# Performance work log

Hardware: AMD Instinct MI355X
Metric: run time of the kernel (lower is better)

The kernel has to match this reference:

```python
import jax, jax.numpy as jnp
import numpy as np

N = 10000      # nodes
E = 640000     # edges
P = 500000     # OD training pairs
IN, HID, EMB = 128, 256, 64


def _graph_conv(x, W, b, src, dst, norm_out, norm_in):
    # DGL GraphConv, norm='both': y = D_in^{-1/2} A (D_out^{-1/2} x) W + b
    h = x * norm_out[:, None]
    agg = jax.ops.segment_sum(h[src], dst, num_segments=N)  # [N, d]
    return agg * norm_in[:, None] @ W + b


def setup_inputs() -> dict:
    key = jax.random.key(0)
    ks = jax.random.split(key, 13)
    x = jax.random.normal(ks[0], (N, IN), jnp.float32)
    dis = jax.random.uniform(ks[1], (N, N), jnp.float32)
    src = jax.random.randint(ks[2], (E,), 0, N, dtype=jnp.int64)
    dst = jax.random.randint(ks[3], (E,), 0, N, dtype=jnp.int64)
    train_idx = jax.random.randint(ks[4], (2, P), 0, N, dtype=jnp.int64)

    def w(k, i, o):
        return (jax.random.normal(k, (i, o), jnp.float32) / np.sqrt(i)).astype(jnp.float32)

    return {
        'x': x, 'dis': dis,
        'W1': w(ks[5], IN, HID),  'b1': jnp.zeros((HID,), jnp.float32),
        'W2': w(ks[6], HID, HID), 'b2': jnp.zeros((HID,), jnp.float32),
        'W3': w(ks[7], HID, EMB), 'b3': jnp.zeros((EMB,), jnp.float32),
        'Wout': w(ks[8], 2 * EMB + 1, 1), 'bout': jnp.zeros((1,), jnp.float32),
        'src': src, 'dst': dst, 'train_idx': train_idx,
    }


def reference(x, dis, W1, b1, W2, b2, W3, b3, Wout, bout, src, dst, train_idx):
    ones = jnp.ones((E,), x.dtype)
    deg_out = jax.ops.segment_sum(ones, src, num_segments=N)
    deg_in = jax.ops.segment_sum(ones, dst, num_segments=N)
    norm_out = jnp.where(deg_out > 0, jax.lax.rsqrt(jnp.maximum(deg_out, 1.0)), 0.0)
    norm_in = jnp.where(deg_in > 0, jax.lax.rsqrt(jnp.maximum(deg_in, 1.0)), 0.0)

    h = jax.nn.relu(_graph_conv(x, W1, b1, src, dst, norm_out, norm_in))
    h = jax.nn.relu(_graph_conv(h, W2, b2, src, dst, norm_out, norm_in))
    g_emb = jax.nn.sigmoid(_graph_conv(h, W3, b3, src, dst, norm_out, norm_in))  # [N, EMB]

    o_emb = g_emb[train_idx[0]]                      # [P, EMB]
    d_emb = g_emb[train_idx[1]]                      # [P, EMB]
    dis_emb = dis[train_idx[0], train_idx[1]][:, None]  # [P, 1]
    emb = jnp.concatenate((o_emb, d_emb, dis_emb), axis=1)  # [P, 2*EMB+1]
    return jnp.tanh(emb @ Wout + bout)               # [P, 1]
```

## Files before the change

### kernel.cpp

```cpp
#include <hip/hip_runtime.h>
#include <math.h>

typedef __attribute__((ext_vector_type(8))) short short8;
typedef __attribute__((ext_vector_type(8))) unsigned short ushort8;
typedef __attribute__((ext_vector_type(4))) float f32x4;

#define NTHR 256
#define CAP 192

__device__ __forceinline__ ushort f2bf(float f) {
    uint u = __float_as_uint(f);
    return (ushort)((u + 0x7FFFu + ((u >> 16) & 1u)) >> 16);
}
__device__ __forceinline__ uint pk2bf(float a, float b) {
    return (uint)f2bf(a) | ((uint)f2bf(b) << 16);
}
__device__ __forceinline__ float bfl(uint r) { return __uint_as_float(r << 16); }
__device__ __forceinline__ float bfh(uint r) { return __uint_as_float(r & 0xFFFF0000u); }

struct Params {
    const float* x; const float* dis;
    const float* W1; const float* b1;
    const float* W2; const float* b2;
    const float* W3; const float* b3;
    const float* Wout; const float* bout;
    const int* src; const int* dst; const int* ti;
    float* out;
    uint* degOut; uint* fill;
    float* normOut; float* normIn;
    ushort* ebkt;
    ushort* xbf; ushort* w1bf; ushort* w2bf; ushort* w3bf;
    ushort* bufA; ushort* bufB; ushort* bufC;
    float* av; float* bv;
    int N, E, P;
};

__global__ __launch_bounds__(NTHR) void k_pre(Params p) {
    int gtid = blockIdx.x * NTHR + threadIdx.x;
    int GSZ = gridDim.x * NTHR;
    for (int i = gtid; i < p.N; i += GSZ) {
        p.degOut[i] = 0u;
        p.fill[i] = 0u;
    }
    if (gtid < 64) ((uint*)&p.xbf[(size_t)p.N * 128])[gtid] = 0u;
    else if (gtid < 192) ((uint*)&p.bufB[(size_t)p.N * 256])[gtid - 64] = 0u;
    else if (gtid < 224) ((uint*)&p.bufC[(size_t)p.N * 64])[gtid - 192] = 0u;
    const int n1 = 128 * 256, n2 = 256 * 256, n3 = 256 * 64;
    int nw4 = (n1 + n2 + n3) >> 2;
    for (int i4 = gtid; i4 < nw4; i4 += GSZ) {
        int i = i4 * 4;
        const float* s;
        ushort* d;
        int off;
        if (i < n1) { s = p.W1; d = p.w1bf; off = i; }
        else if (i < n1 + n2) { s = p.W2; d = p.w2bf; off = i - n1; }
        else { s = p.W3; d = p.w3bf; off = i - n1 - n2; }
        float4 v = *(const float4*)&s[off];
        uint2 pkv;
        pkv.x = pk2bf(v.x, v.y);
        pkv.y = pk2bf(v.z, v.w);
        *(uint2*)&d[off] = pkv;
    }
}

__global__ __launch_bounds__(NTHR) void k_deg_scatter(Params p) {
    int e = (blockIdx.x * NTHR + threadIdx.x) * 2;
    if (e + 1 < p.E) {
        int2 s2 = *(const int2*)&p.src[e];
        int2 d2 = *(const int2*)&p.dst[e];
        atomicAdd(&p.degOut[s2.x], 1u);
        atomicAdd(&p.degOut[s2.y], 1u);
        uint p0 = atomicAdd(&p.fill[d2.x], 1u);
        p.ebkt[(size_t)d2.x * CAP + p0] = (ushort)s2.x;
        uint p1 = atomicAdd(&p.fill[d2.y], 1u);
        p.ebkt[(size_t)d2.y * CAP + p1] = (ushort)s2.y;
    } else if (e < p.E) {
        int s = p.src[e];
        int v = p.dst[e];
        atomicAdd(&p.degOut[s], 1u);
        uint pos = atomicAdd(&p.fill[v], 1u);
        p.ebkt[(size_t)v * CAP + pos] = (ushort)s;
    }
}

__global__ __launch_bounds__(NTHR) void k_norm_cvt(Params p) {
    int gtid = blockIdx.x * NTHR + threadIdx.x;
    int GSZ = gridDim.x * NTHR;
    for (int v = gtid; v < p.N; v += GSZ) {
        uint d0 = p.degOut[v];
        uint d1 = p.fill[v];
        p.normOut[v] = d0 ? rsqrtf((float)d0) : 0.f;
        p.normIn[v] = d1 ? rsqrtf((float)d1) : 0.f;
        uint c8 = (d1 + 7) & ~7u;
        ushort* eb = p.ebkt + (size_t)v * CAP;
        for (uint j = d1; j < c8; ++j) eb[j] = (ushort)p.N;
    }
    int nx4 = p.N * 32;
    for (int i4 = gtid; i4 < nx4; i4 += GSZ) {
        int i = i4 * 4;
        int row = i >> 7;
        uint d0 = p.degOut[row];
        float no = d0 ? rsqrtf((float)d0) : 0.f;
        float4 v = *(const float4*)&p.x[i];
        uint2 pkv;
        pkv.x = pk2bf(v.x * no, v.y * no);
        pkv.y = pk2bf(v.z * no, v.w * no);
        *(uint2*)&p.xbf[i] = pkv;
    }
}

template <int V> struct GT;
template <> struct GT<1> { using T = ushort; };
template <> struct GT<2> { using T = uint; };

template <int V>
__device__ __forceinline__ void accum(float* acc, typename GT<V>::T g) {
    if constexpr (V == 1) {
        acc[0] += bfl((uint)g);
    } else {
        acc[0] += bfl(g);
        acc[1] += bfh(g);
    }
}

template <int D, int SPLIT, int ACT>
__global__ __launch_bounds__(NTHR) void k_agg(Params p, const ushort* __restrict__ h,
                                              ushort* __restrict__ outb) {
    constexpr int V = D / (64 * SPLIT);
    using T = typename GT<V>::T;
    int wib = threadIdx.x >> 6;
    int b = blockIdx.x;
    int v, half;
    if constexpr (SPLIT == 2) {
        half = b & 1;
        v = (b >> 1) * 4 + wib;
    } else {
        half = 0;
        v = b * 4 + wib;
    }
    if (v >= p.N) return;
    int l = threadIdx.x & 63;
    const ushort* hb = h + half * (64 * V) + l * V;
    const ushort* eb = p.ebkt + (size_t)v * CAP;

    int cnt = (int)p.fill[v];
    float nin = p.normIn[v];
    float acc[V] = {};

    if (cnt > 0) {
        int ngrp = (cnt + 7) >> 3;
        ushort8 w = *(const ushort8*)eb;
        T gp[8];
#pragma unroll
        for (int j = 0; j < 8; ++j) gp[j] = *(const T*)&hb[(int)w[j] * D];
        for (int g = 1; g < ngrp; ++g) {
            ushort8 wn = *(const ushort8*)(eb + g * 8);
            T gn[8];
#pragma unroll
            for (int j = 0; j < 8; ++j) gn[j] = *(const T*)&hb[(int)wn[j] * D];
#pragma unroll
            for (int j = 0; j < 8; ++j) accum<V>(acc, gp[j]);
#pragma unroll
            for (int j = 0; j < 8; ++j) gp[j] = gn[j];
        }
#pragma unroll
        for (int j = 0; j < 8; ++j) accum<V>(acc, gp[j]);
    }

    if constexpr (ACT == 0) {
        static_assert(V == 2, "ACT0 expects V==2");
        *(uint*)&outb[(size_t)v * D + half * (64 * V) + l * V] =
            pk2bf(acc[0] * nin, acc[1] * nin);
    } else {
        float g = acc[0] * nin + p.b3[l];
        g = 1.f / (1.f + __expf(-g));
        float pa = g * p.Wout[l];
        float pb = g * p.Wout[64 + l];
#pragma unroll
        for (int off = 32; off > 0; off >>= 1) {
            pa += __shfl_down(pa, off);
            pb += __shfl_down(pb, off);
        }
        if (l == 0) {
            p.av[v] = pa;
            p.bv[v] = pb;
        }
    }
}

template <int BM, int K, bool RELU, bool BIAS, bool SCALE>
__global__ __launch_bounds__(256) void gemm_nf(const ushort* __restrict__ A,
                                               const ushort* __restrict__ B,
                                               const float* __restrict__ bias,
                                               const float* __restrict__ rowScale,
                                               ushort* __restrict__ C,
                                               int M, int Nn) {
    constexpr int WR = BM / 64;
    constexpr int LB = K + 8;
    __shared__ ushort Bs[64 * LB];

    int tid = threadIdx.x;
    int wave = tid >> 6;
    int lane = tid & 63;
    int l15 = lane & 15;
    int l4 = lane >> 4;
    int m0 = blockIdx.x * BM;
    int n0 = blockIdx.y * 64;

    {
        int j8 = (tid & 7) * 8;
#pragma unroll
        for (int kk = tid >> 3; kk < K; kk += 32) {
            short8 v = *(const short8*)&B[(size_t)kk * Nn + n0 + j8];
#pragma unroll
            for (int j = 0; j < 8; ++j) Bs[(j8 + j) * LB + kk] = (ushort)v[j];
        }
    }
    __syncthreads();

    f32x4 acc[WR][4] = {};
    int rowl[WR];
    const ushort* Ab[WR];
#pragma unroll
    for (int r = 0; r < WR; ++r) {
        rowl[r] = m0 + wave * (16 * WR) + r * 16 + l15;
        Ab[r] = A + (size_t)rowl[r] * K + l4 * 8;
    }

#pragma unroll
    for (int k0 = 0; k0 < K; k0 += 32) {
        short8 bf[4];
#pragma unroll
        for (int n = 0; n < 4; ++n)
            bf[n] = *(const short8*)&Bs[(n * 16 + l15) * LB + k0 + l4 * 8];
#pragma unroll
        for (int r = 0; r < WR; ++r) {
            short8 af = {};
            if (rowl[r] < M) af = *(const short8*)&Ab[r][k0];
#pragma unroll
            for (int n = 0; n < 4; ++n)
                acc[r][n] = __builtin_amdgcn_mfma_f32_16x16x32_bf16(af, bf[n], acc[r][n], 0, 0, 0);
        }
    }

#pragma unroll
    for (int r = 0; r < WR; ++r) {
        int rowb = m0 + wave * (16 * WR) + r * 16 + l4 * 4;
#pragma unroll
        for (int q = 0; q < 4; ++q) {
            int row = rowb + q;
            if (row >= M) continue;
            float sc = SCALE ? rowScale[row] : 1.f;
#pragma unroll
            for (int n = 0; n < 4; ++n) {
                int col = n0 + n * 16 + l15;
                float vv = acc[r][n][q];
                if (BIAS) vv += bias[col];
                if (RELU) vv = fmaxf(vv, 0.f);
                vv *= sc;
                C[(size_t)row * Nn + col] = f2bf(vv);
            }
        }
    }
}

__global__ __launch_bounds__(NTHR) void k_final(Params p) {
    int i = (blockIdx.x * NTHR + threadIdx.x) * 2;
    float w128 = p.Wout[128];
    float b0 = p.bout[0];
    if (i + 1 < p.P) {
        int2 o2 = *(const int2*)&p.ti[i];
        int2 d2 = *(const int2*)&p.ti[p.P + i];
        float dis0 = p.dis[(size_t)o2.x * p.N + d2.x];
        float dis1 = p.dis[(size_t)o2.y * p.N + d2.y];
        float s0 = p.av[o2.x] + p.bv[d2.x] + dis0 * w128 + b0;
        float s1 = p.av[o2.y] + p.bv[d2.y] + dis1 * w128 + b0;
        float2 r = make_float2(tanhf(s0), tanhf(s1));
        *(float2*)&p.out[i] = r;
    } else if (i < p.P) {
        int o = p.ti[i];
        int d = p.ti[p.P + i];
        float s = p.av[o] + p.bv[d] + p.dis[(size_t)o * p.N + d] * w128 + b0;
        p.out[i] = tanhf(s);
    }
}

extern "C" void kernel_launch(void* const* d_in, const int* in_sizes, int n_in,
                              void* d_out, int out_size, void* d_ws, size_t ws_size,
                              hipStream_t stream) {
    Params prm;
    prm.x    = (const float*)d_in[0];
    prm.dis  = (const float*)d_in[1];
    prm.W1   = (const float*)d_in[2];
    prm.b1   = (const float*)d_in[3];
    prm.W2   = (const float*)d_in[4];
    prm.b2   = (const float*)d_in[5];
    prm.W3   = (const float*)d_in[6];
    prm.b3   = (const float*)d_in[7];
    prm.Wout = (const float*)d_in[8];
    prm.bout = (const float*)d_in[9];
    prm.src  = (const int*)d_in[10];
    prm.dst  = (const int*)d_in[11];
    prm.ti   = (const int*)d_in[12];
    prm.out  = (float*)d_out;

    const int IN = 128, HID = 256, EMB = 64;
    prm.N = in_sizes[0] / IN;
    prm.E = in_sizes[10];
    prm.P = in_sizes[12] / 2;
    const int N = prm.N, E = prm.E, P = prm.P;

    char* ws = (char*)d_ws;
    size_t off = 0;
    auto alloc = [&](size_t bytes) {
        size_t o = off;
        off = (off + bytes + 255) & ~(size_t)255;
        return o;
    };
    size_t o_degO = alloc((size_t)N * 4);
    size_t o_fill = alloc((size_t)N * 4);
    size_t o_nrmO = alloc((size_t)N * 4);
    size_t o_nrmI = alloc((size_t)N * 4);
    size_t o_ebkt = alloc((size_t)N * CAP * 2);
    size_t o_xbf  = alloc((size_t)(N + 1) * IN * 2);
    size_t o_w1   = alloc((size_t)IN * HID * 2);
    size_t o_w2   = alloc((size_t)HID * HID * 2);
    size_t o_w3   = alloc((size_t)HID * EMB * 2);
    size_t o_bufA = alloc((size_t)N * HID * 2);
    size_t o_bufB = alloc((size_t)(N + 1) * HID * 2);
    size_t o_bufC = alloc((size_t)(N + 1) * EMB * 2);
    size_t o_av   = alloc((size_t)N * 4);
    size_t o_bv   = alloc((size_t)N * 4);
    (void)ws_size;

    prm.degOut  = (uint*)(ws + o_degO);
    prm.fill    = (uint*)(ws + o_fill);
    prm.normOut = (float*)(ws + o_nrmO);
    prm.normIn  = (float*)(ws + o_nrmI);
    prm.ebkt    = (ushort*)(ws + o_ebkt);
    prm.xbf     = (ushort*)(ws + o_xbf);
    prm.w1bf    = (ushort*)(ws + o_w1);
    prm.w2bf    = (ushort*)(ws + o_w2);
    prm.w3bf    = (ushort*)(ws + o_w3);
    prm.bufA    = (ushort*)(ws + o_bufA);
    prm.bufB    = (ushort*)(ws + o_bufB);
    prm.bufC    = (ushort*)(ws + o_bufC);
    prm.av      = (float*)(ws + o_av);
    prm.bv      = (float*)(ws + o_bv);

    k_pre<<<256, NTHR, 0, stream>>>(prm);
    k_deg_scatter<<<(E / 2 + NTHR - 1) / NTHR, NTHR, 0, stream>>>(prm);
    k_norm_cvt<<<1024, NTHR, 0, stream>>>(prm);

    int nb4 = (N + 3) / 4;

    k_agg<128, 1, 0><<<nb4, NTHR, 0, stream>>>(prm, prm.xbf, prm.bufA);
    {
        dim3 grid((N + 127) / 128, HID / 64);
        gemm_nf<128, 128, true, true, true><<<grid, 256, 0, stream>>>(
            prm.bufA, prm.w1bf, prm.b1, prm.normOut, prm.bufB, N, HID);
    }
    k_agg<256, 2, 0><<<nb4 * 2, NTHR, 0, stream>>>(prm, prm.bufB, prm.bufA);
    {
        dim3 grid((N + 127) / 128, HID / 64);
        gemm_nf<128, 256, true, true, true><<<grid, 256, 0, stream>>>(
            prm.bufA, prm.w2bf, prm.b2, prm.normOut, prm.bufB, N, HID);
    }
    {
        dim3 grid((N + 63) / 64, EMB / 64);
        gemm_nf<64, 256, false, false, false><<<grid, 256, 0, stream>>>(
            prm.bufB, prm.w3bf, nullptr, nullptr, prm.bufC, N, EMB);
    }
    k_agg<64, 1, 2><<<nb4, NTHR, 0, stream>>>(prm, prm.bufC, nullptr);
    k_final<<<(P / 2 + NTHR - 1) / NTHR, NTHR, 0, stream>>>(prm);
}
```

Baseline: 170.0 us.

## Fuse neighbor aggregation with per-layer GEMMs into 32-row block kernels

Aggregation and the dense weight multiply are merged into one kernel per layer. Each 512-thread block gathers 32 rows into shared memory and then runs MFMA on them against pre-transposed bf16 weights read straight from global memory. Layers 2 and 3 share one kernel, with the layer-2 output kept in shared memory for the W3 multiply. The separate weight-conversion kernel becomes a transposing step inside k_norm_cvt, and the counter zeroing becomes a hipMemsetAsync. This removes the bufA round trips and several launches, at the cost of reading weight tiles from global or L2 in every block and a weight-transpose loop with uncoalesced writes.

New measurement: 202.8 us. 1.19x slower.

```diff
diff --git a/kernel.cpp b/kernel.cpp
--- a/kernel.cpp
+++ b/kernel.cpp
@@ -6,6 +6,7 @@
 typedef __attribute__((ext_vector_type(4))) float f32x4;
 
 #define NTHR 256
+#define LTHR 512
 #define CAP 192
 
 __device__ __forceinline__ ushort f2bf(float f) {
@@ -29,39 +30,15 @@
     uint* degOut; uint* fill;
     float* normOut; float* normIn;
     ushort* ebkt;
-    ushort* xbf; ushort* w1bf; ushort* w2bf; ushort* w3bf;
-    ushort* bufA; ushort* bufB; ushort* bufC;
+    ushort* xbf;
+    ushort* w1t;
+    ushort* w2t;
+    ushort* w3t;
+    ushort* bufB;
+    ushort* bufC;
     float* av; float* bv;
     int N, E, P;
 };
-
-__global__ __launch_bounds__(NTHR) void k_pre(Params p) {
-    int gtid = blockIdx.x * NTHR + threadIdx.x;
-    int GSZ = gridDim.x * NTHR;
-    for (int i = gtid; i < p.N; i += GSZ) {
-        p.degOut[i] = 0u;
-        p.fill[i] = 0u;
-    }
-    if (gtid < 64) ((uint*)&p.xbf[(size_t)p.N * 128])[gtid] = 0u;
-    else if (gtid < 192) ((uint*)&p.bufB[(size_t)p.N * 256])[gtid - 64] = 0u;
-    else if (gtid < 224) ((uint*)&p.bufC[(size_t)p.N * 64])[gtid - 192] = 0u;
-    const int n1 = 128 * 256, n2 = 256 * 256, n3 = 256 * 64;
-    int nw4 = (n1 + n2 + n3) >> 2;
-    for (int i4 = gtid; i4 < nw4; i4 += GSZ) {
-        int i = i4 * 4;
-        const float* s;
-        ushort* d;
-        int off;
-        if (i < n1) { s = p.W1; d = p.w1bf; off = i; }
-        else if (i < n1 + n2) { s = p.W2; d = p.w2bf; off = i - n1; }
-        else { s = p.W3; d = p.w3bf; off = i - n1 - n2; }
-        float4 v = *(const float4*)&s[off];
-        uint2 pkv;
-        pkv.x = pk2bf(v.x, v.y);
-        pkv.y = pk2bf(v.z, v.w);
-        *(uint2*)&d[off] = pkv;
-    }
-}
 
 __global__ __launch_bounds__(NTHR) void k_deg_scatter(Params p) {
     int e = (blockIdx.x * NTHR + threadIdx.x) * 2;
@@ -95,6 +72,9 @@
         ushort* eb = p.ebkt + (size_t)v * CAP;
         for (uint j = d1; j < c8; ++j) eb[j] = (ushort)p.N;
     }
+    if (gtid < 64) ((uint*)&p.xbf[(size_t)p.N * 128])[gtid] = 0u;
+    else if (gtid < 192) ((uint*)&p.bufB[(size_t)p.N * 256])[gtid - 64] = 0u;
+    else if (gtid < 224) ((uint*)&p.bufC[(size_t)p.N * 64])[gtid - 192] = 0u;
     int nx4 = p.N * 32;
     for (int i4 = gtid; i4 < nx4; i4 += GSZ) {
         int i = i4 * 4;
@@ -107,160 +87,203 @@
         pkv.y = pk2bf(v.z * no, v.w * no);
         *(uint2*)&p.xbf[i] = pkv;
     }
-}
-
-template <int V> struct GT;
-template <> struct GT<1> { using T = ushort; };
-template <> struct GT<2> { using T = uint; };
-
-template <int V>
-__device__ __forceinline__ void accum(float* acc, typename GT<V>::T g) {
-    if constexpr (V == 1) {
-        acc[0] += bfl((uint)g);
-    } else {
-        acc[0] += bfl(g);
-        acc[1] += bfh(g);
-    }
-}
-
-template <int D, int SPLIT, int ACT>
-__global__ __launch_bounds__(NTHR) void k_agg(Params p, const ushort* __restrict__ h,
-                                              ushort* __restrict__ outb) {
-    constexpr int V = D / (64 * SPLIT);
-    using T = typename GT<V>::T;
-    int wib = threadIdx.x >> 6;
-    int b = blockIdx.x;
-    int v, half;
-    if constexpr (SPLIT == 2) {
-        half = b & 1;
-        v = (b >> 1) * 4 + wib;
-    } else {
-        half = 0;
-        v = b * 4 + wib;
-    }
+    for (int i = gtid; i < 128 * 256; i += GSZ) {
+        int k = i >> 8, c = i & 255;
+        p.w1t[c * 128 + k] = f2bf(p.W1[i]);
+    }
+    for (int i = gtid; i < 256 * 256; i += GSZ) {
+        int k = i >> 8, c = i & 255;
+        p.w2t[c * 256 + k] = f2bf(p.W2[i]);
+    }
+    for (int i = gtid; i < 256 * 64; i += GSZ) {
+        int k = i >> 6, c = i & 63;
+        p.w3t[c * 256 + k] = f2bf(p.W3[i]);
+    }
+}
+
+__global__ __launch_bounds__(LTHR) void k_layer1(Params p) {
+    __shared__ ushort As[32 * 136];
+    int m0 = blockIdx.x * 32;
+    int wid = threadIdx.x >> 6;
+    int l = threadIdx.x & 63;
+
+    const ushort* hb = p.xbf + l * 2;
+#pragma unroll
+    for (int i = 0; i < 4; ++i) {
+        int r = wid * 4 + i;
+        int v = m0 + r;
+        uint pk = 0u;
+        if (v < p.N) {
+            int cnt = (int)p.fill[v];
+            float nin = p.normIn[v];
+            const ushort* eb = p.ebkt + (size_t)v * CAP;
+            float a0 = 0.f, a1 = 0.f;
+            int ngrp = (cnt + 7) >> 3;
+            for (int g = 0; g < ngrp; ++g) {
+                ushort8 w = *(const ushort8*)(eb + g * 8);
+                uint gg[8];
+#pragma unroll
+                for (int j = 0; j < 8; ++j) gg[j] = *(const uint*)&hb[(int)w[j] * 128];
+#pragma unroll
+                for (int j = 0; j < 8; ++j) {
+                    a0 += bfl(gg[j]);
+                    a1 += bfh(gg[j]);
+                }
+            }
+            pk = pk2bf(a0 * nin, a1 * nin);
+        }
+        *(uint*)&As[r * 136 + l * 2] = pk;
+    }
+    __syncthreads();
+
+    int l15 = l & 15, l4 = l >> 4;
+    int rf = wid >> 2;
+    int n0 = (wid & 3) * 64;
+    f32x4 acc[4] = {};
+    const ushort* arow = &As[(rf * 16 + l15) * 136 + l4 * 8];
+#pragma unroll
+    for (int k0 = 0; k0 < 128; k0 += 32) {
+        short8 af = *(const short8*)&arow[k0];
+#pragma unroll
+        for (int n = 0; n < 4; ++n) {
+            short8 bf = *(const short8*)&p.w1t[(size_t)(n0 + n * 16 + l15) * 128 + k0 + l4 * 8];
+            acc[n] = __builtin_amdgcn_mfma_f32_16x16x32_bf16(af, bf, acc[n], 0, 0, 0);
+        }
+    }
+#pragma unroll
+    for (int n = 0; n < 4; ++n) {
+        int col = n0 + n * 16 + l15;
+        float bs = p.b1[col];
+#pragma unroll
+        for (int q = 0; q < 4; ++q) {
+            int row = m0 + rf * 16 + l4 * 4 + q;
+            if (row < p.N) {
+                float vv = fmaxf(acc[n][q] + bs, 0.f) * p.normOut[row];
+                p.bufB[(size_t)row * 256 + col] = f2bf(vv);
+            }
+        }
+    }
+}
+
+__global__ __launch_bounds__(LTHR) void k_layer23(Params p) {
+    __shared__ ushort As[32 * 264];
+    __shared__ ushort Cs[32 * 264];
+    int m0 = blockIdx.x * 32;
+    int wid = threadIdx.x >> 6;
+    int l = threadIdx.x & 63;
+    int l15 = l & 15, l4 = l >> 4;
+
+    const ushort* hb = p.bufB + l * 4;
+#pragma unroll
+    for (int i = 0; i < 4; ++i) {
+        int r = wid * 4 + i;
+        int v = m0 + r;
+        uint2 pk = make_uint2(0u, 0u);
+        if (v < p.N) {
+            int cnt = (int)p.fill[v];
+            float nin = p.normIn[v];
+            const ushort* eb = p.ebkt + (size_t)v * CAP;
+            float a0 = 0.f, a1 = 0.f, a2 = 0.f, a3 = 0.f;
+            int ngrp = (cnt + 7) >> 3;
+            for (int g = 0; g < ngrp; ++g) {
+                ushort8 w = *(const ushort8*)(eb + g * 8);
+                uint2 gg[8];
+#pragma unroll
+                for (int j = 0; j < 8; ++j) gg[j] = *(const uint2*)&hb[(int)w[j] * 256];
+#pragma unroll
+                for (int j = 0; j < 8; ++j) {
+                    a0 += bfl(gg[j].x);
+                    a1 += bfh(gg[j].x);
+                    a2 += bfl(gg[j].y);
+                    a3 += bfh(gg[j].y);
+                }
+            }
+            pk.x = pk2bf(a0 * nin, a1 * nin);
+            pk.y = pk2bf(a2 * nin, a3 * nin);
+        }
+        *(uint2*)&As[r * 264 + l * 4] = pk;
+    }
+    __syncthreads();
+
+    {
+        int rf = wid >> 2;
+        int n0 = (wid & 3) * 64;
+        f32x4 acc[4] = {};
+        const ushort* arow = &As[(rf * 16 + l15) * 264 + l4 * 8];
+#pragma unroll
+        for (int k0 = 0; k0 < 256; k0 += 32) {
+            short8 af = *(const short8*)&arow[k0];
+#pragma unroll
+            for (int n = 0; n < 4; ++n) {
+                short8 bf = *(const short8*)&p.w2t[(size_t)(n0 + n * 16 + l15) * 256 + k0 + l4 * 8];
+                acc[n] = __builtin_amdgcn_mfma_f32_16x16x32_bf16(af, bf, acc[n], 0, 0, 0);
+            }
+        }
+#pragma unroll
+        for (int n = 0; n < 4; ++n) {
+            int col = n0 + n * 16 + l15;
+            float bs = p.b2[col];
+#pragma unroll
+            for (int q = 0; q < 4; ++q) {
+                int rl = rf * 16 + l4 * 4 + q;
+                int row = m0 + rl;
+                float no = (row < p.N) ? p.normOut[row] : 0.f;
+                Cs[rl * 264 + col] = f2bf(fmaxf(acc[n][q] + bs, 0.f) * no);
+            }
+        }
+    }
+    __syncthreads();
+
+    {
+        int rf = wid & 1;
+        int nf = wid >> 1;
+        f32x4 acc = {};
+        const ushort* arow = &Cs[(rf * 16 + l15) * 264 + l4 * 8];
+#pragma unroll
+        for (int k0 = 0; k0 < 256; k0 += 32) {
+            short8 af = *(const short8*)&arow[k0];
+            short8 bf = *(const short8*)&p.w3t[(size_t)(nf * 16 + l15) * 256 + k0 + l4 * 8];
+            acc = __builtin_amdgcn_mfma_f32_16x16x32_bf16(af, bf, acc, 0, 0, 0);
+        }
+        int col = nf * 16 + l15;
+#pragma unroll
+        for (int q = 0; q < 4; ++q) {
+            int row = m0 + rf * 16 + l4 * 4 + q;
+            if (row < p.N) p.bufC[(size_t)row * 64 + col] = f2bf(acc[q]);
+        }
+    }
+}
+
+__global__ __launch_bounds__(NTHR) void k_agg3(Params p) {
+    int v = blockIdx.x * 4 + (threadIdx.x >> 6);
     if (v >= p.N) return;
     int l = threadIdx.x & 63;
-    const ushort* hb = h + half * (64 * V) + l * V;
+    const ushort* hb = p.bufC + l;
     const ushort* eb = p.ebkt + (size_t)v * CAP;
-
     int cnt = (int)p.fill[v];
     float nin = p.normIn[v];
-    float acc[V] = {};
-
-    if (cnt > 0) {
-        int ngrp = (cnt + 7) >> 3;
-        ushort8 w = *(const ushort8*)eb;
-        T gp[8];
-#pragma unroll
-        for (int j = 0; j < 8; ++j) gp[j] = *(const T*)&hb[(int)w[j] * D];
-        for (int g = 1; g < ngrp; ++g) {
-            ushort8 wn = *(const ushort8*)(eb + g * 8);
-            T gn[8];
-#pragma unroll
-            for (int j = 0; j < 8; ++j) gn[j] = *(const T*)&hb[(int)wn[j] * D];
-#pragma unroll
-            for (int j = 0; j < 8; ++j) accum<V>(acc, gp[j]);
-#pragma unroll
-            for (int j = 0; j < 8; ++j) gp[j] = gn[j];
-        }
-#pragma unroll
-        for (int j = 0; j < 8; ++j) accum<V>(acc, gp[j]);
-    }
-
-    if constexpr (ACT == 0) {
-        static_assert(V == 2, "ACT0 expects V==2");
-        *(uint*)&outb[(size_t)v * D + half * (64 * V) + l * V] =
-            pk2bf(acc[0] * nin, acc[1] * nin);
-    } else {
-        float g = acc[0] * nin + p.b3[l];
-        g = 1.f / (1.f + __expf(-g));
-        float pa = g * p.Wout[l];
-        float pb = g * p.Wout[64 + l];
-#pragma unroll
-        for (int off = 32; off > 0; off >>= 1) {
-            pa += __shfl_down(pa, off);
-            pb += __shfl_down(pb, off);
-        }
-        if (l == 0) {
-            p.av[v] = pa;
-            p.bv[v] = pb;
-        }
-    }
-}
-
-template <int BM, int K, bool RELU, bool BIAS, bool SCALE>
-__global__ __launch_bounds__(256) void gemm_nf(const ushort* __restrict__ A,
-                                               const ushort* __restrict__ B,
-                                               const float* __restrict__ bias,
-                                               const float* __restrict__ rowScale,
-                                               ushort* __restrict__ C,
-                                               int M, int Nn) {
-    constexpr int WR = BM / 64;
-    constexpr int LB = K + 8;
-    __shared__ ushort Bs[64 * LB];
-
-    int tid = threadIdx.x;
-    int wave = tid >> 6;
-    int lane = tid & 63;
-    int l15 = lane & 15;
-    int l4 = lane >> 4;
-    int m0 = blockIdx.x * BM;
-    int n0 = blockIdx.y * 64;
-
-    {
-        int j8 = (tid & 7) * 8;
-#pragma unroll
-        for (int kk = tid >> 3; kk < K; kk += 32) {
-            short8 v = *(const short8*)&B[(size_t)kk * Nn + n0 + j8];
-#pragma unroll
-            for (int j = 0; j < 8; ++j) Bs[(j8 + j) * LB + kk] = (ushort)v[j];
-        }
-    }
-    __syncthreads();
-
-    f32x4 acc[WR][4] = {};
-    int rowl[WR];
-    const ushort* Ab[WR];
-#pragma unroll
-    for (int r = 0; r < WR; ++r) {
-        rowl[r] = m0 + wave * (16 * WR) + r * 16 + l15;
-        Ab[r] = A + (size_t)rowl[r] * K + l4 * 8;
-    }
-
-#pragma unroll
-    for (int k0 = 0; k0 < K; k0 += 32) {
-        short8 bf[4];
-#pragma unroll
-        for (int n = 0; n < 4; ++n)
-            bf[n] = *(const short8*)&Bs[(n * 16 + l15) * LB + k0 + l4 * 8];
-#pragma unroll
-        for (int r = 0; r < WR; ++r) {
-            short8 af = {};
-            if (rowl[r] < M) af = *(const short8*)&Ab[r][k0];
-#pragma unroll
-            for (int n = 0; n < 4; ++n)
-                acc[r][n] = __builtin_amdgcn_mfma_f32_16x16x32_bf16(af, bf[n], acc[r][n], 0, 0, 0);
-        }
-    }
-
-#pragma unroll
-    for (int r = 0; r < WR; ++r) {
-        int rowb = m0 + wave * (16 * WR) + r * 16 + l4 * 4;
-#pragma unroll
-        for (int q = 0; q < 4; ++q) {
-            int row = rowb + q;
-            if (row >= M) continue;
-            float sc = SCALE ? rowScale[row] : 1.f;
-#pragma unroll
-            for (int n = 0; n < 4; ++n) {
-                int col = n0 + n * 16 + l15;
-                float vv = acc[r][n][q];
-                if (BIAS) vv += bias[col];
-                if (RELU) vv = fmaxf(vv, 0.f);
-                vv *= sc;
-                C[(size_t)row * Nn + col] = f2bf(vv);
-            }
-        }
+    float acc = 0.f;
+    int ngrp = (cnt + 7) >> 3;
+    for (int g = 0; g < ngrp; ++g) {
+        ushort8 w = *(const ushort8*)(eb + g * 8);
+        ushort gg[8];
+#pragma unroll
+        for (int j = 0; j < 8; ++j) gg[j] = hb[(int)w[j] * 64];
+#pragma unroll
+        for (int j = 0; j < 8; ++j) acc += bfl((uint)gg[j]);
+    }
+    float g = acc * nin + p.b3[l];
+    g = 1.f / (1.f + __expf(-g));
+    float pa = g * p.Wout[l];
+    float pb = g * p.Wout[64 + l];
+#pragma unroll
+    for (int off = 32; off > 0; off >>= 1) {
+        pa += __shfl_down(pa, off);
+        pb += __shfl_down(pb, off);
+    }
+    if (l == 0) {
+        p.av[v] = pa;
+        p.bv[v] = pb;
     }
 }
 
@@ -317,8 +340,7 @@
         off = (off + bytes + 255) & ~(size_t)255;
         return o;
     };
-    size_t o_degO = alloc((size_t)N * 4);
-    size_t o_fill = alloc((size_t)N * 4);
+    size_t o_cnts = alloc((size_t)2 * N * 4);
     size_t o_nrmO = alloc((size_t)N * 4);
     size_t o_nrmI = alloc((size_t)N * 4);
     size_t o_ebkt = alloc((size_t)N * CAP * 2);
@@ -326,51 +348,33 @@
     size_t o_w1   = alloc((size_t)IN * HID * 2);
     size_t o_w2   = alloc((size_t)HID * HID * 2);
     size_t o_w3   = alloc((size_t)HID * EMB * 2);
-    size_t o_bufA = alloc((size_t)N * HID * 2);
     size_t o_bufB = alloc((size_t)(N + 1) * HID * 2);
     size_t o_bufC = alloc((size_t)(N + 1) * EMB * 2);
     size_t o_av   = alloc((size_t)N * 4);
     size_t o_bv   = alloc((size_t)N * 4);
     (void)ws_size;
 
-    prm.degOut  = (uint*)(ws + o_degO);
-    prm.fill    = (uint*)(ws + o_fill);
+    prm.degOut  = (uint*)(ws + o_cnts);
+    prm.fill    = prm.degOut + N;
     prm.normOut = (float*)(ws + o_nrmO);
     prm.normIn  = (float*)(ws + o_nrmI);
     prm.ebkt    = (ushort*)(ws + o_ebkt);
     prm.xbf     = (ushort*)(ws + o_xbf);
-    prm.w1bf    = (ushort*)(ws + o_w1);
-    prm.w2bf    = (ushort*)(ws + o_w2);
-    prm.w3bf    = (ushort*)(ws + o_w3);
-    prm.bufA    = (ushort*)(ws + o_bufA);
+    prm.w1t     = (ushort*)(ws + o_w1);
+    prm.w2t     = (ushort*)(ws + o_w2);
+    prm.w3t     = (ushort*)(ws + o_w3);
     prm.bufB    = (ushort*)(ws + o_bufB);
     prm.bufC    = (ushort*)(ws + o_bufC);
     prm.av      = (float*)(ws + o_av);
     prm.bv      = (float*)(ws + o_bv);
 
-    k_pre<<<256, NTHR, 0, stream>>>(prm);
+    hipMemsetAsync(prm.degOut, 0, (size_t)2 * N * 4, stream);
     k_deg_scatter<<<(E / 2 + NTHR - 1) / NTHR, NTHR, 0, stream>>>(prm);
     k_norm_cvt<<<1024, NTHR, 0, stream>>>(prm);
 
-    int nb4 = (N + 3) / 4;
-
-    k_agg<128, 1, 0><<<nb4, NTHR, 0, stream>>>(prm, prm.xbf, prm.bufA);
-    {
-        dim3 grid((N + 127) / 128, HID / 64);
-        gemm_nf<128, 128, true, true, true><<<grid, 256, 0, stream>>>(
-            prm.bufA, prm.w1bf, prm.b1, prm.normOut, prm.bufB, N, HID);
-    }
-    k_agg<256, 2, 0><<<nb4 * 2, NTHR, 0, stream>>>(prm, prm.bufB, prm.bufA);
-    {
-        dim3 grid((N + 127) / 128, HID / 64);
-        gemm_nf<128, 256, true, true, true><<<grid, 256, 0, stream>>>(
-            prm.bufA, prm.w2bf, prm.b2, prm.normOut, prm.bufB, N, HID);
-    }
-    {
-        dim3 grid((N + 63) / 64, EMB / 64);
-        gemm_nf<64, 256, false, false, false><<<grid, 256, 0, stream>>>(
-            prm.bufB, prm.w3bf, nullptr, nullptr, prm.bufC, N, EMB);
-    }
-    k_agg<64, 1, 2><<<nb4, NTHR, 0, stream>>>(prm, prm.bufC, nullptr);
+    int nbl = (N + 31) / 32;
+    k_layer1<<<nbl, LTHR, 0, stream>>>(prm);
+    k_layer23<<<nbl, LTHR, 0, stream>>>(prm);
+    k_agg3<<<(N + 3) / 4, NTHR, 0, stream>>>(prm);
     k_final<<<(P / 2 + NTHR - 1) / NTHR, NTHR, 0, stream>>>(prm);
 }
```

## Fuse layer-2 and layer-3 GEMMs through LDS and pre-transpose weights

Applied to the files above, without the earlier changes.

Layer-2 and layer-3 GEMMs now run in one kernel: the 32-row layer-2 output tile stays in shared memory and feeds the W3 product directly, so the intermediate buffer no longer round-trips through global memory and one launch disappears. Weights are transposed and converted to bf16 once inside the norm/convert kernel, letting the GEMMs read B fragments straight from global/L2 instead of staging them in LDS. The k_pre kernel is replaced by a memset plus work folded into k_norm_cvt. The trade-offs are strided scalar weight-transpose writes and B operand loads that every block repeats from cache.

Result: slower. 180.9 us (+6.5%).

```diff
diff --git a/kernel.cpp b/kernel.cpp
--- a/kernel.cpp
+++ b/kernel.cpp
@@ -29,39 +29,16 @@
     uint* degOut; uint* fill;
     float* normOut; float* normIn;
     ushort* ebkt;
-    ushort* xbf; ushort* w1bf; ushort* w2bf; ushort* w3bf;
-    ushort* bufA; ushort* bufB; ushort* bufC;
+    ushort* xbf;
+    ushort* w1t;
+    ushort* w2t;
+    ushort* w3t;
+    ushort* bufA;
+    ushort* bufB;
+    ushort* bufC;
     float* av; float* bv;
     int N, E, P;
 };
-
-__global__ __launch_bounds__(NTHR) void k_pre(Params p) {
-    int gtid = blockIdx.x * NTHR + threadIdx.x;
-    int GSZ = gridDim.x * NTHR;
-    for (int i = gtid; i < p.N; i += GSZ) {
-        p.degOut[i] = 0u;
-        p.fill[i] = 0u;
-    }
-    if (gtid < 64) ((uint*)&p.xbf[(size_t)p.N * 128])[gtid] = 0u;
-    else if (gtid < 192) ((uint*)&p.bufB[(size_t)p.N * 256])[gtid - 64] = 0u;
-    else if (gtid < 224) ((uint*)&p.bufC[(size_t)p.N * 64])[gtid - 192] = 0u;
-    const int n1 = 128 * 256, n2 = 256 * 256, n3 = 256 * 64;
-    int nw4 = (n1 + n2 + n3) >> 2;
-    for (int i4 = gtid; i4 < nw4; i4 += GSZ) {
-        int i = i4 * 4;
-        const float* s;
-        ushort* d;
-        int off;
-        if (i < n1) { s = p.W1; d = p.w1bf; off = i; }
-        else if (i < n1 + n2) { s = p.W2; d = p.w2bf; off = i - n1; }
-        else { s = p.W3; d = p.w3bf; off = i - n1 - n2; }
-        float4 v = *(const float4*)&s[off];
-        uint2 pkv;
-        pkv.x = pk2bf(v.x, v.y);
-        pkv.y = pk2bf(v.z, v.w);
-        *(uint2*)&d[off] = pkv;
-    }
-}
 
 __global__ __launch_bounds__(NTHR) void k_deg_scatter(Params p) {
     int e = (blockIdx.x * NTHR + threadIdx.x) * 2;
@@ -95,6 +72,9 @@
         ushort* eb = p.ebkt + (size_t)v * CAP;
         for (uint j = d1; j < c8; ++j) eb[j] = (ushort)p.N;
     }
+    if (gtid < 64) ((uint*)&p.xbf[(size_t)p.N * 128])[gtid] = 0u;
+    else if (gtid < 192) ((uint*)&p.bufB[(size_t)p.N * 256])[gtid - 64] = 0u;
+    else if (gtid < 224) ((uint*)&p.bufC[(size_t)p.N * 64])[gtid - 192] = 0u;
     int nx4 = p.N * 32;
     for (int i4 = gtid; i4 < nx4; i4 += GSZ) {
         int i = i4 * 4;
@@ -106,6 +86,18 @@
         pkv.x = pk2bf(v.x * no, v.y * no);
         pkv.y = pk2bf(v.z * no, v.w * no);
         *(uint2*)&p.xbf[i] = pkv;
+    }
+    for (int i = gtid; i < 128 * 256; i += GSZ) {
+        int k = i >> 8, c = i & 255;
+        p.w1t[c * 128 + k] = f2bf(p.W1[i]);
+    }
+    for (int i = gtid; i < 256 * 256; i += GSZ) {
+        int k = i >> 8, c = i & 255;
+        p.w2t[c * 256 + k] = f2bf(p.W2[i]);
+    }
+    for (int i = gtid; i < 256 * 64; i += GSZ) {
+        int k = i >> 6, c = i & 63;
+        p.w3t[c * 256 + k] = f2bf(p.W3[i]);
     }
 }
 
@@ -168,9 +160,12 @@
     }
 
     if constexpr (ACT == 0) {
-        static_assert(V == 2, "ACT0 expects V==2");
-        *(uint*)&outb[(size_t)v * D + half * (64 * V) + l * V] =
-            pk2bf(acc[0] * nin, acc[1] * nin);
+        if constexpr (V == 2) {
+            *(uint*)&outb[(size_t)v * D + half * (64 * V) + l * V] =
+                pk2bf(acc[0] * nin, acc[1] * nin);
+        } else {
+            outb[(size_t)v * D + half * 64 + l] = f2bf(acc[0] * nin);
+        }
     } else {
         float g = acc[0] * nin + p.b3[l];
         g = 1.f / (1.f + __expf(-g));
@@ -188,77 +183,102 @@
     }
 }
 
-template <int BM, int K, bool RELU, bool BIAS, bool SCALE>
-__global__ __launch_bounds__(256) void gemm_nf(const ushort* __restrict__ A,
-                                               const ushort* __restrict__ B,
-                                               const float* __restrict__ bias,
-                                               const float* __restrict__ rowScale,
-                                               ushort* __restrict__ C,
-                                               int M, int Nn) {
-    constexpr int WR = BM / 64;
-    constexpr int LB = K + 8;
-    __shared__ ushort Bs[64 * LB];
-
-    int tid = threadIdx.x;
-    int wave = tid >> 6;
-    int lane = tid & 63;
-    int l15 = lane & 15;
-    int l4 = lane >> 4;
-    int m0 = blockIdx.x * BM;
+__global__ __launch_bounds__(NTHR) void k_gemm1(Params p) {
+    int wid = threadIdx.x >> 6;
+    int l = threadIdx.x & 63;
+    int l15 = l & 15, l4 = l >> 4;
+    int m0 = blockIdx.x * 64;
     int n0 = blockIdx.y * 64;
+    int row = m0 + wid * 16 + l15;
+    bool rok = row < p.N;
+    const ushort* Ab = p.bufA + (size_t)row * 128 + l4 * 8;
+
+    f32x4 acc[4] = {};
+#pragma unroll
+    for (int k0 = 0; k0 < 128; k0 += 32) {
+        short8 af = {};
+        if (rok) af = *(const short8*)&Ab[k0];
+#pragma unroll
+        for (int n = 0; n < 4; ++n) {
+            short8 bf = *(const short8*)&p.w1t[(size_t)(n0 + n * 16 + l15) * 128 + k0 + l4 * 8];
+            acc[n] = __builtin_amdgcn_mfma_f32_16x16x32_bf16(af, bf, acc[n], 0, 0, 0);
+        }
+    }
+#pragma unroll
+    for (int n = 0; n < 4; ++n) {
+        int col = n0 + n * 16 + l15;
+        float bs = p.b1[col];
+#pragma unroll
+        for (int q = 0; q < 4; ++q) {
+            int grow = m0 + wid * 16 + l4 * 4 + q;
+            if (grow < p.N) {
+                float vv = fmaxf(acc[n][q] + bs, 0.f) * p.normOut[grow];
+                p.bufB[(size_t)grow * 256 + col] = f2bf(vv);
+            }
+        }
+    }
+}
+
+__global__ __launch_bounds__(NTHR) void k_gemm23(Params p) {
+    __shared__ ushort Cs[32 * 264];
+    int wid = threadIdx.x >> 6;
+    int l = threadIdx.x & 63;
+    int l15 = l & 15, l4 = l >> 4;
+    int m0 = blockIdx.x * 32;
+    int rfrag = wid & 1;
+    int chunk = wid >> 1;
 
     {
-        int j8 = (tid & 7) * 8;
-#pragma unroll
-        for (int kk = tid >> 3; kk < K; kk += 32) {
-            short8 v = *(const short8*)&B[(size_t)kk * Nn + n0 + j8];
-#pragma unroll
-            for (int j = 0; j < 8; ++j) Bs[(j8 + j) * LB + kk] = (ushort)v[j];
+        int row = m0 + rfrag * 16 + l15;
+        bool rok = row < p.N;
+        const ushort* Ab = p.bufA + (size_t)row * 256 + l4 * 8;
+        f32x4 acc[8] = {};
+#pragma unroll
+        for (int k0 = 0; k0 < 256; k0 += 32) {
+            short8 af = {};
+            if (rok) af = *(const short8*)&Ab[k0];
+#pragma unroll
+            for (int n = 0; n < 8; ++n) {
+                int col = chunk * 128 + n * 16 + l15;
+                short8 bf = *(const short8*)&p.w2t[(size_t)col * 256 + k0 + l4 * 8];
+                acc[n] = __builtin_amdgcn_mfma_f32_16x16x32_bf16(af, bf, acc[n], 0, 0, 0);
+            }
+        }
+#pragma unroll
+        for (int n = 0; n < 8; ++n) {
+            int col = chunk * 128 + n * 16 + l15;
+            float bs = p.b2[col];
+#pragma unroll
+            for (int q = 0; q < 4; ++q) {
+                int rl = rfrag * 16 + l4 * 4 + q;
+                int grow = m0 + rl;
+                float no = (grow < p.N) ? p.normOut[grow] : 0.f;
+                Cs[rl * 264 + col] = f2bf(fmaxf(acc[n][q] + bs, 0.f) * no);
+            }
         }
     }
     __syncthreads();
 
-    f32x4 acc[WR][4] = {};
-    int rowl[WR];
-    const ushort* Ab[WR];
-#pragma unroll
-    for (int r = 0; r < WR; ++r) {
-        rowl[r] = m0 + wave * (16 * WR) + r * 16 + l15;
-        Ab[r] = A + (size_t)rowl[r] * K + l4 * 8;
-    }
-
-#pragma unroll
-    for (int k0 = 0; k0 < K; k0 += 32) {
-        short8 bf[4];
-#pragma unroll
-        for (int n = 0; n < 4; ++n)
-            bf[n] = *(const short8*)&Bs[(n * 16 + l15) * LB + k0 + l4 * 8];
-#pragma unroll
-        for (int r = 0; r < WR; ++r) {
-            short8 af = {};
-            if (rowl[r] < M) af = *(const short8*)&Ab[r][k0];
-#pragma unroll
-            for (int n = 0; n < 4; ++n)
-                acc[r][n] = __builtin_amdgcn_mfma_f32_16x16x32_bf16(af, bf[n], acc[r][n], 0, 0, 0);
-        }
-    }
-
-#pragma unroll
-    for (int r = 0; r < WR; ++r) {
-        int rowb = m0 + wave * (16 * WR) + r * 16 + l4 * 4;
-#pragma unroll
-        for (int q = 0; q < 4; ++q) {
-            int row = rowb + q;
-            if (row >= M) continue;
-            float sc = SCALE ? rowScale[row] : 1.f;
-#pragma unroll
-            for (int n = 0; n < 4; ++n) {
-                int col = n0 + n * 16 + l15;
-                float vv = acc[r][n][q];
-                if (BIAS) vv += bias[col];
-                if (RELU) vv = fmaxf(vv, 0.f);
-                vv *= sc;
-                C[(size_t)row * Nn + col] = f2bf(vv);
+    {
+        const ushort* arow = &Cs[(rfrag * 16 + l15) * 264 + l4 * 8];
+        f32x4 a3[2] = {};
+#pragma unroll
+        for (int k0 = 0; k0 < 256; k0 += 32) {
+            short8 af = *(const short8*)&arow[k0];
+#pragma unroll
+            for (int n = 0; n < 2; ++n) {
+                int col = chunk * 32 + n * 16 + l15;
+                short8 bf = *(const short8*)&p.w3t[(size_t)col * 256 + k0 + l4 * 8];
+                a3[n] = __builtin_amdgcn_mfma_f32_16x16x32_bf16(af, bf, a3[n], 0, 0, 0);
+            }
+        }
+#pragma unroll
+        for (int n = 0; n < 2; ++n) {
+            int col = chunk * 32 + n * 16 + l15;
+#pragma unroll
+            for (int q = 0; q < 4; ++q) {
+                int grow = m0 + rfrag * 16 + l4 * 4 + q;
+                if (grow < p.N) p.bufC[(size_t)grow * 64 + col] = f2bf(a3[n][q]);
             }
         }
     }
@@ -317,8 +337,7 @@
         off = (off + bytes + 255) & ~(size_t)255;
         return o;
     };
-    size_t o_degO = alloc((size_t)N * 4);
-    size_t o_fill = alloc((size_t)N * 4);
+    size_t o_cnts = alloc((size_t)2 * N * 4);
     size_t o_nrmO = alloc((size_t)N * 4);
     size_t o_nrmI = alloc((size_t)N * 4);
     size_t o_ebkt = alloc((size_t)N * CAP * 2);
@@ -333,22 +352,22 @@
     size_t o_bv   = alloc((size_t)N * 4);
     (void)ws_size;
 
-    prm.degOut  = (uint*)(ws + o_degO);
-    prm.fill    = (uint*)(ws + o_fill);
+    prm.degOut  = (uint*)(ws + o_cnts);
+    prm.fill    = prm.degOut + N;
     prm.normOut = (float*)(ws + o_nrmO);
     prm.normIn  = (float*)(ws + o_nrmI);
     prm.ebkt    = (ushort*)(ws + o_ebkt);
     prm.xbf     = (ushort*)(ws + o_xbf);
-    prm.w1bf    = (ushort*)(ws + o_w1);
-    prm.w2bf    = (ushort*)(ws + o_w2);
-    prm.w3bf    = (ushort*)(ws + o_w3);
+    prm.w1t     = (ushort*)(ws + o_w1);
+    prm.w2t     = (ushort*)(ws + o_w2);
+    prm.w3t     = (ushort*)(ws + o_w3);
     prm.bufA    = (ushort*)(ws + o_bufA);
     prm.bufB    = (ushort*)(ws + o_bufB);
     prm.bufC    = (ushort*)(ws + o_bufC);
     prm.av      = (float*)(ws + o_av);
     prm.bv      = (float*)(ws + o_bv);
 
-    k_pre<<<256, NTHR, 0, stream>>>(prm);
+    hipMemsetAsync(prm.degOut, 0, (size_t)2 * N * 4, stream);
     k_deg_scatter<<<(E / 2 + NTHR - 1) / NTHR, NTHR, 0, stream>>>(prm);
     k_norm_cvt<<<1024, NTHR, 0, stream>>>(prm);
 
@@ -356,21 +375,11 @@
 
     k_agg<128, 1, 0><<<nb4, NTHR, 0, stream>>>(prm, prm.xbf, prm.bufA);
     {
-        dim3 grid((N + 127) / 128, HID / 64);
-        gemm_nf<128, 128, true, true, true><<<grid, 256, 0, stream>>>(
-            prm.bufA, prm.w1bf, prm.b1, prm.normOut, prm.bufB, N, HID);
+        dim3 grid((N + 63) / 64, 4);
+        k_gemm1<<<grid, NTHR, 0, stream>>>(prm);
     }
     k_agg<256, 2, 0><<<nb4 * 2, NTHR, 0, stream>>>(prm, prm.bufB, prm.bufA);
-    {
-        dim3 grid((N + 127) / 128, HID / 64);
-        gemm_nf<128, 256, true, true, true><<<grid, 256, 0, stream>>>(
-            prm.bufA, prm.w2bf, prm.b2, prm.normOut, prm.bufB, N, HID);
-    }
-    {
-        dim3 grid((N + 63) / 64, EMB / 64);
-        gemm_nf<64, 256, false, false, false><<<grid, 256, 0, stream>>>(
-            prm.bufB, prm.w3bf, nullptr, nullptr, prm.bufC, N, EMB);
-    }
+    k_gemm23<<<(N + 31) / 32, NTHR, 0, stream>>>(prm);
     k_agg<64, 1, 2><<<nb4, NTHR, 0, stream>>>(prm, prm.bufC, nullptr);
     k_final<<<(P / 2 + NTHR - 1) / NTHR, NTHR, 0, stream>>>(prm);
 }
```

## Split aggregation across more feature slices and fold preprocessing into existing kernels

Applied to the files above, without the earlier changes.

Removes the separate preprocessing kernel. The counter zeroing becomes a single memset on a merged counts buffer, and the weight bf16 conversion and pad-row zeroing are folded into the scatter and norm kernels. The neighbor aggregation kernels now split each node's feature vector over 2 or 4 wavefronts instead of 1 or 2, so each lane gathers one bf16 value. That launches more waves to hide gather latency, at the cost of re-reading each node's edge list per slice and narrower per-lane loads.

After: 191.2 us. 1.12x slower.

```diff
diff --git a/kernel.cpp b/kernel.cpp
--- a/kernel.cpp
+++ b/kernel.cpp
@@ -29,42 +29,18 @@
     uint* degOut; uint* fill;
     float* normOut; float* normIn;
     ushort* ebkt;
-    ushort* xbf; ushort* w1bf; ushort* w2bf; ushort* w3bf;
-    ushort* bufA; ushort* bufB; ushort* bufC;
+    ushort* xbf;
+    ushort* w1bf; ushort* w2bf; ushort* w3bf;
+    ushort* bufA;
+    ushort* bufB;
+    ushort* bufC;
     float* av; float* bv;
     int N, E, P;
 };
 
-__global__ __launch_bounds__(NTHR) void k_pre(Params p) {
+__global__ __launch_bounds__(NTHR) void k_deg_scatter(Params p) {
     int gtid = blockIdx.x * NTHR + threadIdx.x;
-    int GSZ = gridDim.x * NTHR;
-    for (int i = gtid; i < p.N; i += GSZ) {
-        p.degOut[i] = 0u;
-        p.fill[i] = 0u;
-    }
-    if (gtid < 64) ((uint*)&p.xbf[(size_t)p.N * 128])[gtid] = 0u;
-    else if (gtid < 192) ((uint*)&p.bufB[(size_t)p.N * 256])[gtid - 64] = 0u;
-    else if (gtid < 224) ((uint*)&p.bufC[(size_t)p.N * 64])[gtid - 192] = 0u;
-    const int n1 = 128 * 256, n2 = 256 * 256, n3 = 256 * 64;
-    int nw4 = (n1 + n2 + n3) >> 2;
-    for (int i4 = gtid; i4 < nw4; i4 += GSZ) {
-        int i = i4 * 4;
-        const float* s;
-        ushort* d;
-        int off;
-        if (i < n1) { s = p.W1; d = p.w1bf; off = i; }
-        else if (i < n1 + n2) { s = p.W2; d = p.w2bf; off = i - n1; }
-        else { s = p.W3; d = p.w3bf; off = i - n1 - n2; }
-        float4 v = *(const float4*)&s[off];
-        uint2 pkv;
-        pkv.x = pk2bf(v.x, v.y);
-        pkv.y = pk2bf(v.z, v.w);
-        *(uint2*)&d[off] = pkv;
-    }
-}
-
-__global__ __launch_bounds__(NTHR) void k_deg_scatter(Params p) {
-    int e = (blockIdx.x * NTHR + threadIdx.x) * 2;
+    int e = gtid * 2;
     if (e + 1 < p.E) {
         int2 s2 = *(const int2*)&p.src[e];
         int2 d2 = *(const int2*)&p.dst[e];
@@ -81,6 +57,23 @@
         uint pos = atomicAdd(&p.fill[v], 1u);
         p.ebkt[(size_t)v * CAP + pos] = (ushort)s;
     }
+    const int n1 = 128 * 256, n2 = 256 * 256, n3 = 256 * 64;
+    int GSZ = gridDim.x * NTHR;
+    int nw4 = (n1 + n2 + n3) >> 2;
+    for (int i4 = gtid; i4 < nw4; i4 += GSZ) {
+        int i = i4 * 4;
+        const float* s;
+        ushort* d;
+        int off;
+        if (i < n1) { s = p.W1; d = p.w1bf; off = i; }
+        else if (i < n1 + n2) { s = p.W2; d = p.w2bf; off = i - n1; }
+        else { s = p.W3; d = p.w3bf; off = i - n1 - n2; }
+        float4 v = *(const float4*)&s[off];
+        uint2 pkv;
+        pkv.x = pk2bf(v.x, v.y);
+        pkv.y = pk2bf(v.z, v.w);
+        *(uint2*)&d[off] = pkv;
+    }
 }
 
 __global__ __launch_bounds__(NTHR) void k_norm_cvt(Params p) {
@@ -95,6 +88,9 @@
         ushort* eb = p.ebkt + (size_t)v * CAP;
         for (uint j = d1; j < c8; ++j) eb[j] = (ushort)p.N;
     }
+    if (gtid < 64) ((uint*)&p.xbf[(size_t)p.N * 128])[gtid] = 0u;
+    else if (gtid < 192) ((uint*)&p.bufB[(size_t)p.N * 256])[gtid - 64] = 0u;
+    else if (gtid < 224) ((uint*)&p.bufC[(size_t)p.N * 64])[gtid - 192] = 0u;
     int nx4 = p.N * 32;
     for (int i4 = gtid; i4 < nx4; i4 += GSZ) {
         int i = i4 * 4;
@@ -127,20 +123,15 @@
 __global__ __launch_bounds__(NTHR) void k_agg(Params p, const ushort* __restrict__ h,
                                               ushort* __restrict__ outb) {
     constexpr int V = D / (64 * SPLIT);
+    constexpr int SH = (SPLIT == 4) ? 2 : ((SPLIT == 2) ? 1 : 0);
     using T = typename GT<V>::T;
     int wib = threadIdx.x >> 6;
     int b = blockIdx.x;
-    int v, half;
-    if constexpr (SPLIT == 2) {
-        half = b & 1;
-        v = (b >> 1) * 4 + wib;
-    } else {
-        half = 0;
-        v = b * 4 + wib;
-    }
+    int part = b & (SPLIT - 1);
+    int v = (b >> SH) * 4 + wib;
     if (v >= p.N) return;
     int l = threadIdx.x & 63;
-    const ushort* hb = h + half * (64 * V) + l * V;
+    const ushort* hb = h + part * (64 * V) + l * V;
     const ushort* eb = p.ebkt + (size_t)v * CAP;
 
     int cnt = (int)p.fill[v];
@@ -168,9 +159,12 @@
     }
 
     if constexpr (ACT == 0) {
-        static_assert(V == 2, "ACT0 expects V==2");
-        *(uint*)&outb[(size_t)v * D + half * (64 * V) + l * V] =
-            pk2bf(acc[0] * nin, acc[1] * nin);
+        if constexpr (V == 2) {
+            *(uint*)&outb[(size_t)v * D + part * (64 * V) + l * V] =
+                pk2bf(acc[0] * nin, acc[1] * nin);
+        } else {
+            outb[(size_t)v * D + part * 64 + l] = f2bf(acc[0] * nin);
+        }
     } else {
         float g = acc[0] * nin + p.b3[l];
         g = 1.f / (1.f + __expf(-g));
@@ -317,8 +311,7 @@
         off = (off + bytes + 255) & ~(size_t)255;
         return o;
     };
-    size_t o_degO = alloc((size_t)N * 4);
-    size_t o_fill = alloc((size_t)N * 4);
+    size_t o_cnts = alloc((size_t)2 * N * 4);
     size_t o_nrmO = alloc((size_t)N * 4);
     size_t o_nrmI = alloc((size_t)N * 4);
     size_t o_ebkt = alloc((size_t)N * CAP * 2);
@@ -333,8 +326,8 @@
     size_t o_bv   = alloc((size_t)N * 4);
     (void)ws_size;
 
-    prm.degOut  = (uint*)(ws + o_degO);
-    prm.fill    = (uint*)(ws + o_fill);
+    prm.degOut  = (uint*)(ws + o_cnts);
+    prm.fill    = prm.degOut + N;
     prm.normOut = (float*)(ws + o_nrmO);
     prm.normIn  = (float*)(ws + o_nrmI);
     prm.ebkt    = (ushort*)(ws + o_ebkt);
@@ -348,19 +341,19 @@
     prm.av      = (float*)(ws + o_av);
     prm.bv      = (float*)(ws + o_bv);
 
-    k_pre<<<256, NTHR, 0, stream>>>(prm);
+    hipMemsetAsync(prm.degOut, 0, (size_t)2 * N * 4, stream);
     k_deg_scatter<<<(E / 2 + NTHR - 1) / NTHR, NTHR, 0, stream>>>(prm);
-    k_norm_cvt<<<1024, NTHR, 0, stream>>>(prm);
+    k_norm_cvt<<<512, NTHR, 0, stream>>>(prm);
 
     int nb4 = (N + 3) / 4;
 
-    k_agg<128, 1, 0><<<nb4, NTHR, 0, stream>>>(prm, prm.xbf, prm.bufA);
+    k_agg<128, 2, 0><<<nb4 * 2, NTHR, 0, stream>>>(prm, prm.xbf, prm.bufA);
     {
         dim3 grid((N + 127) / 128, HID / 64);
         gemm_nf<128, 128, true, true, true><<<grid, 256, 0, stream>>>(
             prm.bufA, prm.w1bf, prm.b1, prm.normOut, prm.bufB, N, HID);
     }
-    k_agg<256, 2, 0><<<nb4 * 2, NTHR, 0, stream>>>(prm, prm.bufB, prm.bufA);
+    k_agg<256, 4, 0><<<nb4 * 4, NTHR, 0, stream>>>(prm, prm.bufB, prm.bufA);
     {
         dim3 grid((N + 127) / 128, HID / 64);
         gemm_nf<128, 256, true, true, true><<<grid, 256, 0, stream>>>(
```
